# Optimization experiments

Measured on AMD Instinct MI355X. Metric: run time of the kernel, lower is better.

The kernel has to match this reference:

```python
import jax, jax.numpy as jnp
import numpy as np

B, T = 8, 8192
D_X, D_H, D_K, D_V = 256, 512, 128, 128
RES_DIMS = [128, 128, 128, 128]
R = sum(RES_DIMS)
MEM_SLOTS, EP_TOPK = 256, 8
LN_EPS = 1e-5


def _ln(x, g, b):
    m = x.mean(-1, keepdims=True)
    v = ((x - m) ** 2).mean(-1, keepdims=True)
    return (x - m) * jax.lax.rsqrt(v + LN_EPS) * g + b


def _l2norm(x, eps=1e-8):
    return x / jnp.maximum(jnp.linalg.norm(x, axis=-1, keepdims=True), eps)


def setup_inputs() -> dict:
    key = jax.random.key(0)
    ks = jax.random.split(key, 12)
    def w(k, shape):  # xavier-ish scaling
        return jax.random.normal(k, shape, jnp.float32) * (shape[-1] ** -0.5)
    return dict(
        x_seq=jax.random.normal(ks[0], (B, T, D_X), jnp.float32),
        Wx_w=w(ks[1], (R, D_X)), Wx_b=jnp.zeros((R,), jnp.float32),
        Wh_w=w(ks[2], (R, D_H)),
        res_alpha=jnp.full((len(RES_DIMS),), -1.0, jnp.float32),
        A_scale=jnp.ones((D_H,), jnp.float32),
        B_w=w(ks[3], (D_H, R)),
        U_w=w(ks[4], (D_H, D_X)), U_b=jnp.zeros((D_H,), jnp.float32),
        fftn_g=jnp.ones((D_H,), jnp.float32), fftn_b=jnp.zeros((D_H,), jnp.float32),
        fftp_w=w(ks[5], (D_H, D_H)), fftp_b=jnp.zeros((D_H,), jnp.float32),
        fft_mix=jnp.asarray(0.5, jnp.float32),
        mix_logit=jnp.asarray(0.0, jnp.float32),
        key_w=w(ks[6], (D_K, R + D_X)), key_b=jnp.zeros((D_K,), jnp.float32),
        val_w=w(ks[7], (D_V, D_H)), val_b=jnp.zeros((D_V,), jnp.float32),
        rm_w=w(ks[8], (D_H, D_V)), rm_b=jnp.zeros((D_H,), jnp.float32),
        rn_g=jnp.ones((R,), jnp.float32), rn_b=jnp.zeros((R,), jnp.float32),
        mem_keys=jax.random.normal(ks[9], (B, MEM_SLOTS, D_K), jnp.float32),
        mem_vals=jax.random.normal(ks[10], (B, MEM_SLOTS, D_K), jnp.float32),
        heb_H=jax.random.normal(ks[11], (B, D_K, D_V), jnp.float32) * 0.1,
    )


def reference(x_seq, Wx_w, Wx_b, Wh_w, res_alpha, A_scale, B_w, U_w, U_b,
              fftn_g, fftn_b, fftp_w, fftp_b, fft_mix, mix_logit,
              key_w, key_b, val_w, val_b, rm_w, rm_b, rn_g, rn_b,
              mem_keys, mem_vals, heb_H):
    b = x_seq.shape[0]
    seg_index = np.repeat(np.arange(len(RES_DIMS)), RES_DIMS)  # static (R,)
    h_prev = jnp.zeros((b, D_H), x_seq.dtype)  # h0 = None
    r_prev = jnp.zeros((b, R), x_seq.dtype)    # r0 = None

    # reservoir update (fully parallel over T since h_prev/r_prev are broadcast)
    Wx = jnp.einsum('btx,rx->btr', x_seq, Wx_w) + Wx_b
    Wh = (h_prev @ Wh_w.T)[:, None, :]                    # (B,1,R), no bias in fwd
    alpha = jax.nn.sigmoid(res_alpha)[seg_index]          # (R,)
    r_seq = alpha * r_prev[:, None, :] + (1.0 - alpha) * jnp.tanh(Wx + Wh)
    r_seq = _ln(r_seq, rn_g, rn_b)

    # core state
    Ah = A_scale * h_prev[:, None, :]
    Bh = jnp.einsum('btr,hr->bth', r_seq, B_w)
    Uh = jnp.einsum('btx,hx->bth', x_seq, U_w) + U_b
    h_tilde = jax.nn.gelu(Ah + Bh + Uh, approximate=False)

    # FFT feature mixing
    h_norm = _ln(h_tilde, fftn_g, fftn_b)
    s = jax.nn.sigmoid(fft_mix)
    h_freq = jnp.fft.rfft(h_norm, n=D_H, axis=-1, norm='ortho')
    h_ifft = jnp.fft.irfft(h_freq * s, n=D_H, axis=-1, norm='ortho')
    h_fft_out = jnp.einsum('bth,oh->bto', h_ifft, fftp_w) + fftp_b
    hs = (1.0 - s) * h_tilde + s * h_fft_out

    # memory recall (once per sequence, batched)
    k = jnp.einsum('btf,kf->btk', jnp.concatenate([r_seq, x_seq], axis=-1), key_w) + key_b
    v = jnp.einsum('bth,vh->btv', hs, val_w) + val_b  # as in original (used for auto_write)
    c = _l2norm(k)
    q = c.mean(axis=1)                                # (B,d_k)

    # episodic: cosine top-k over slots, softmax-weighted value read
    kn = _l2norm(mem_keys)
    sim = jnp.einsum('bk,bmk->bm', _l2norm(q), kn)
    top_sim, top_idx = jax.lax.top_k(sim, EP_TOPK)
    w_att = jax.nn.softmax(top_sim, axis=-1)
    vals = jnp.take_along_axis(mem_vals, top_idx[..., None], axis=1)  # (B,topk,d_v)
    v_hat = jnp.einsum('bk,bkv->bv', w_att, vals)

    # hebbian: linear associative read from per-batch outer-product memory
    v_hebb = jnp.einsum('bk,bkv->bv', q, heb_H)

    mix = jax.nn.sigmoid(mix_logit)
    v_comb = mix * v_hat + (1.0 - mix) * v_hebb
    h_mem = v_comb @ rm_w.T + rm_b                    # (B,d_h)
    hs = hs + 0.5 * h_mem[:, None, :]
    return hs, r_seq
```

## Files before the change

### kernel.cpp

```cpp
#include <hip/hip_runtime.h>
#include <cmath>


typedef __attribute__((ext_vector_type(8)))  short short8;
typedef __attribute__((ext_vector_type(16))) float f32x16;

__device__ __forceinline__ unsigned short f2bf(float f) {
  union { float f; unsigned u; } v; v.f = f;
  unsigned r = v.u + 0x7FFF + ((v.u >> 16) & 1);
  return (unsigned short)(r >> 16);
}
__device__ __forceinline__ float bf2f(unsigned short h) {
  union { unsigned u; float f; } v; v.u = ((unsigned)h) << 16; return v.f;
}
__device__ __forceinline__ f32x16 mfma16(short8 a, short8 b, f32x16 c) {
  return __builtin_amdgcn_mfma_f32_32x32x16_bf16(a, b, c, 0, 0, 0);
}
__device__ __forceinline__ void glds1k(const unsigned short* g, short* l, int lane) {
  typedef const __attribute__((address_space(1))) unsigned int* gp_t;
  typedef __attribute__((address_space(3))) unsigned int* lp_t;
  __builtin_amdgcn_global_load_lds((gp_t)(const void*)(g + lane * 8),
                                   (lp_t)(void*)l, 16, 0, 0);
}
__device__ __forceinline__ void barrier_lgkm() {
  asm volatile("s_waitcnt lgkmcnt(0)" ::: "memory");
  __builtin_amdgcn_s_barrier();
  __builtin_amdgcn_sched_barrier(0);
}

__global__ __launch_bounds__(256) void k_wconv(
    const float* __restrict__ wx, const float* __restrict__ key,
    const float* __restrict__ bw, const float* __restrict__ uw,
    const float* __restrict__ fftpw, const float* __restrict__ fg,
    unsigned short* __restrict__ wxp, unsigned short* __restrict__ keyp,
    unsigned short* __restrict__ bwp, unsigned short* __restrict__ uwp,
    unsigned short* __restrict__ fftps) {
  int i = blockIdx.x * 256 + threadIdx.x;
  if (i >= 884736) return;
  float v; int n, k, N; unsigned short* dst;
  if (i < 131072)      { int j = i;          N = 512; k = j & 255; n = j >> 8; v = wx[j];  dst = wxp; }
  else if (i < 229376) { int j = i - 131072; N = 128; k = j % 768; n = j / 768; v = key[j]; dst = keyp; }
  else if (i < 491520) { int j = i - 229376; N = 512; k = j & 511; n = j >> 9; v = bw[j];  dst = bwp; }
  else if (i < 622592) { int j = i - 491520; N = 512; k = j & 255; n = j >> 8; v = uw[j];  dst = uwp; }
  else                 { int j = i - 622592; N = 512; k = j & 511; n = j >> 9; v = fftpw[j] * fg[k]; dst = fftps; }
  dst[(k >> 5) * (N * 32) + ((k >> 3) & 3) * (N * 8) + n * 8 + (k & 7)] = f2bf(v);
}

__global__ __launch_bounds__(512, 4) void k_rseq(
    const float* __restrict__ x, const unsigned short* __restrict__ wxp,
    const float* __restrict__ wxb, const float* __restrict__ resa,
    const float* __restrict__ rng, const float* __restrict__ rnb,
    float* __restrict__ rout) {
  __shared__ short sA[2][1024];
  __shared__ float red[640];
  const int t = threadIdx.x, w = t >> 6, lane = t & 63, lr = lane & 31, lh = lane >> 5;
  const int m0 = blockIdx.x * 32;

  f32x16 acc[2];
#pragma unroll
  for (int ni = 0; ni < 2; ++ni)
#pragma unroll
    for (int e = 0; e < 16; ++e) acc[ni][e] = 0.f;

  short8 b0[4], b1[4];
  float2 a0, a1;

  auto loadB = [&](int sn, short8 (&bd)[4]) {
#pragma unroll
    for (int kh = 0; kh < 2; ++kh)
#pragma unroll
      for (int ni = 0; ni < 2; ++ni)
        bd[kh * 2 + ni] = *reinterpret_cast<const short8*>(
            wxp + (size_t)sn * 16384 + (kh * 2 + lh) * 4096 + (64 * w + 32 * ni + lr) * 8);
  };
  auto loadAct = [&](int sn, float2& ad) {
    int row = t >> 4, kq2 = t & 15;
    ad = *reinterpret_cast<const float2*>(x + (size_t)(m0 + row) * 256 + sn * 32 + kq2 * 2);
  };
  auto writeAct = [&](const float2& ad, int buf) {
    int row = t >> 4, kq2 = t & 15;
    unsigned p = (unsigned)f2bf(ad.x) | ((unsigned)f2bf(ad.y) << 16);
    *reinterpret_cast<unsigned*>(&sA[buf][(kq2 >> 2) * 256 + row * 8 + (kq2 & 3) * 2]) = p;
  };
  auto mfstep = [&](int buf, short8 (&bc)[4]) {
    short8 af[2];
#pragma unroll
    for (int kh = 0; kh < 2; ++kh)
      af[kh] = *reinterpret_cast<const short8*>(&sA[buf][(kh * 2 + lh) * 256 + lr * 8]);
    __builtin_amdgcn_s_setprio(1);
#pragma unroll
    for (int kh = 0; kh < 2; ++kh)
#pragma unroll
      for (int ni = 0; ni < 2; ++ni)
        acc[ni] = mfma16(af[kh], bc[kh * 2 + ni], acc[ni]);
    __builtin_amdgcn_s_setprio(0);
  };

  const int NS = 8;
  loadAct(0, a0);
  loadB(0, b0);
  loadAct(1, a1);
  writeAct(a0, 0);
  barrier_lgkm();
  for (int s = 0; s < NS; s += 2) {
    if (s + 1 < NS) loadB(s + 1, b1);
    if (s + 2 < NS) loadAct(s + 2, a0);
    mfstep(s & 1, b0);
    if (s + 1 < NS) writeAct(a1, (s + 1) & 1);
    barrier_lgkm();
    if (s + 2 < NS) loadB(s + 2, b0);
    if (s + 3 < NS) loadAct(s + 3, a1);
    mfstep((s + 1) & 1, b1);
    if (s + 2 < NS) writeAct(a0, s & 1);
    barrier_lgkm();
  }

#pragma unroll
  for (int ni = 0; ni < 2; ++ni) {
    int col = 64 * w + 32 * ni + lr;
    float al = 1.f / (1.f + expf(-resa[col >> 7]));
    float oma = 1.f - al, bbv = wxb[col];
#pragma unroll
    for (int r = 0; r < 16; ++r)
      acc[ni][r] = oma * tanhf(acc[ni][r] + bbv);
  }
#pragma unroll
  for (int r = 0; r < 16; ++r) {
    float s1 = acc[0][r] + acc[1][r];
    float s2 = acc[0][r] * acc[0][r] + acc[1][r] * acc[1][r];
#pragma unroll
    for (int m = 1; m <= 16; m <<= 1) { s1 += __shfl_xor(s1, m); s2 += __shfl_xor(s2, m); }
    int rl = (r & 3) + 8 * (r >> 2) + 4 * lh;
    if (lr == r) { red[w * 32 + rl] = s1; red[256 + w * 32 + rl] = s2; }
  }
  __syncthreads();
  if (t < 32) {
    float s1 = 0.f, s2 = 0.f;
#pragma unroll
    for (int n = 0; n < 8; ++n) { s1 += red[n * 32 + t]; s2 += red[256 + n * 32 + t]; }
    float mean = s1 * (1.f / 512.f);
    float var = s2 * (1.f / 512.f) - mean * mean;
    float rstd = rsqrtf(var + 1e-5f);
    red[512 + t * 2] = mean;
    red[512 + t * 2 + 1] = rstd;
  }
  __syncthreads();
#pragma unroll
  for (int q = 0; q < 4; ++q) {
    float4 stA = *reinterpret_cast<float4*>(&red[512 + (8 * q + 4 * lh) * 2]);
    float4 stB = *reinterpret_cast<float4*>(&red[512 + (8 * q + 4 * lh) * 2 + 4]);
    float mean[4] = {stA.x, stA.z, stB.x, stB.z};
    float rstd[4] = {stA.y, stA.w, stB.y, stB.w};
#pragma unroll
    for (int ni = 0; ni < 2; ++ni) {
      int col = 64 * w + 32 * ni + lr;
      float g = rng[col], bbv = rnb[col];
#pragma unroll
      for (int e = 0; e < 4; ++e) {
        int r = 4 * q + e;
        int grow = m0 + 8 * q + 4 * lh + e;
        rout[(size_t)grow * 512 + col] = (acc[ni][r] - mean[e]) * rstd[e] * g + bbv;
      }
    }
  }
}

__global__ __launch_bounds__(512, 2) void k_kq(
    const float* __restrict__ rseq, const float* __restrict__ x,
    const unsigned short* __restrict__ keyp, const float* __restrict__ keyb,
    float* __restrict__ partial) {
  __shared__ short sA[2][4096];
  const int t = threadIdx.x, w = t >> 6, lane = t & 63, lr = lane & 31, lh = lane >> 5;
  const int mw = w >> 1, nw = w & 1;
  const int m0 = blockIdx.x * 128;

  f32x16 acc[2];
#pragma unroll
  for (int ni = 0; ni < 2; ++ni)
#pragma unroll
    for (int e = 0; e < 16; ++e) acc[ni][e] = 0.f;

  short8 b0[4], b1[4];
  float4 a0[2], a1[2];

  auto loadB = [&](int sn, short8 (&bd)[4]) {
#pragma unroll
    for (int kh = 0; kh < 2; ++kh)
#pragma unroll
      for (int ni = 0; ni < 2; ++ni)
        bd[kh * 2 + ni] = *reinterpret_cast<const short8*>(
            keyp + (size_t)sn * 4096 + (kh * 2 + lh) * 1024 + (64 * nw + 32 * ni + lr) * 8);
  };
  auto loadAct = [&](int sn, float4 (&ad)[2]) {
    const float* src; int str, kb;
    if (sn < 16) { src = rseq; str = 512; kb = sn * 32; }
    else         { src = x;    str = 256; kb = (sn - 16) * 32; }
#pragma unroll
    for (int i = 0; i < 2; ++i) {
      int c = t + i * 512, row = c >> 3, kq = c & 7;
      ad[i] = *reinterpret_cast<const float4*>(src + (size_t)(m0 + row) * str + kb + kq * 4);
    }
  };
  auto writeAct = [&](const float4 (&ad)[2], int buf) {
#pragma unroll
    for (int i = 0; i < 2; ++i) {
      int c = t + i * 512, row = c >> 3, kq = c & 7;
      uint2 p;
      p.x = (unsigned)f2bf(ad[i].x) | ((unsigned)f2bf(ad[i].y) << 16);
      p.y = (unsigned)f2bf(ad[i].z) | ((unsigned)f2bf(ad[i].w) << 16);
      *reinterpret_cast<uint2*>(&sA[buf][(kq >> 1) * 1024 + row * 8 + (kq & 1) * 4]) = p;
    }
  };
  auto mfstep = [&](int buf, short8 (&bc)[4]) {
    short8 af[2];
#pragma unroll
    for (int kh = 0; kh < 2; ++kh)
      af[kh] = *reinterpret_cast<const short8*>(
          &sA[buf][(kh * 2 + lh) * 1024 + (32 * mw + lr) * 8]);
    __builtin_amdgcn_s_setprio(1);
#pragma unroll
    for (int kh = 0; kh < 2; ++kh)
#pragma unroll
      for (int ni = 0; ni < 2; ++ni)
        acc[ni] = mfma16(af[kh], bc[kh * 2 + ni], acc[ni]);
    __builtin_amdgcn_s_setprio(0);
  };

  const int NS = 24;
  loadAct(0, a0);
  loadB(0, b0);
  loadAct(1, a1);
  writeAct(a0, 0);
  barrier_lgkm();
  for (int s = 0; s < NS; s += 2) {
    if (s + 1 < NS) loadB(s + 1, b1);
    if (s + 2 < NS) loadAct(s + 2, a0);
    mfstep(s & 1, b0);
    if (s + 1 < NS) writeAct(a1, (s + 1) & 1);
    barrier_lgkm();
    if (s + 2 < NS) loadB(s + 2, b0);
    if (s + 3 < NS) loadAct(s + 3, a1);
    mfstep((s + 1) & 1, b1);
    if (s + 2 < NS) writeAct(a0, s & 1);
    barrier_lgkm();
  }

#pragma unroll
  for (int ni = 0; ni < 2; ++ni) {
    int col = 64 * nw + 32 * ni + lr;
    float bbv = keyb[col];
#pragma unroll
    for (int r = 0; r < 16; ++r) acc[ni][r] += bbv;
  }
  float* red = reinterpret_cast<float*>(sA);
#pragma unroll
  for (int r = 0; r < 16; ++r) {
    float s2 = acc[0][r] * acc[0][r] + acc[1][r] * acc[1][r];
#pragma unroll
    for (int m = 1; m <= 16; m <<= 1) s2 += __shfl_xor(s2, m);
    int rl = (r & 3) + 8 * (r >> 2) + 4 * lh;
    if (lr == r) red[(nw * 4 + mw) * 32 + rl] = s2;
  }
  __syncthreads();
  if (t < 128) {
    int ms = t >> 5, rl = t & 31;
    float s = red[(0 * 4 + ms) * 32 + rl] + red[(4 + ms) * 32 + rl];
    red[256 + ms * 32 + rl] = 1.f / fmaxf(sqrtf(s), 1e-8f);
  }
  __syncthreads();
  float p0 = 0.f, p1 = 0.f;
#pragma unroll
  for (int q = 0; q < 4; ++q) {
    float4 sc4 = *reinterpret_cast<float4*>(&red[256 + mw * 32 + 8 * q + 4 * lh]);
    float sc[4] = {sc4.x, sc4.y, sc4.z, sc4.w};
#pragma unroll
    for (int e = 0; e < 4; ++e) {
      int r = 4 * q + e;
      p0 += acc[0][r] * sc[e];
      p1 += acc[1][r] * sc[e];
    }
  }
  p0 += __shfl_xor(p0, 32);
  p1 += __shfl_xor(p1, 32);
  if (lh == 0) {
    red[384 + mw * 128 + 64 * nw + lr]      = p0;
    red[384 + mw * 128 + 64 * nw + 32 + lr] = p1;
  }
  __syncthreads();
  if (t < 128)
    partial[(size_t)blockIdx.x * 128 + t] =
        red[384 + t] + red[384 + 128 + t] + red[384 + 256 + t] + red[384 + 384 + t];
}

__global__ __launch_bounds__(256) void k_qred(const float* __restrict__ partial,
                                              float* __restrict__ q_ws) {
  int gid = blockIdx.x * 256 + threadIdx.x;
  int b = gid >> 7, c = gid & 127;
  float s = 0.f;
  for (int i = 0; i < 64; ++i) s += partial[(size_t)(b * 64 + i) * 128 + c];
  q_ws[gid] = s * (1.f / 8192.f);
}

__global__ __launch_bounds__(256) void k_cvec(const float* __restrict__ fb,
                                              const float* __restrict__ fftpw,
                                              float* __restrict__ cvec) {
  int o = blockIdx.x * 256 + threadIdx.x;
  const float* w = fftpw + (size_t)o * 512;
  float s = 0.f;
  for (int k = 0; k < 512; ++k) s += fb[k] * w[k];
  cvec[o] = s;
}

__global__ __launch_bounds__(256) void k_mem(
    const float* __restrict__ q_ws, const float* __restrict__ mkeys,
    const float* __restrict__ mvals, const float* __restrict__ hebH,
    const float* __restrict__ rmw, const float* __restrict__ rmb,
    const float* __restrict__ mixl, float* __restrict__ hm) {
  const int b = blockIdx.x, t = threadIdx.x;
  __shared__ float qv[128];
  __shared__ float ssim[256];
  __shared__ float red[256];
  __shared__ float tval[8];
  __shared__ int tidx[8];
  __shared__ float wsm[8];
  __shared__ float vcs[128];

  if (t < 128) qv[t] = q_ws[b * 128 + t];
  __syncthreads();
  red[t] = (t < 128) ? qv[t] * qv[t] : 0.f;
  __syncthreads();
  for (int s = 128; s > 0; s >>= 1) {
    if (t < s) red[t] += red[t + s];
    __syncthreads();
  }
  float qsc = 1.f / fmaxf(sqrtf(red[0]), 1e-8f);
  {
    const float* mk = mkeys + ((size_t)b * 256 + t) * 128;
    float dot = 0.f, ms = 0.f;
    for (int k = 0; k < 128; ++k) { float mv = mk[k]; dot += qv[k] * mv; ms += mv * mv; }
    ssim[t] = dot * qsc / fmaxf(sqrtf(ms), 1e-8f);
  }
  __syncthreads();
  for (int it = 0; it < 8; ++it) {
    if (t < 64) {
      float bv = -1e30f; int bi = 0;
#pragma unroll
      for (int u = 0; u < 4; ++u) {
        int m = t * 4 + u;
        float v = ssim[m];
        if (v > bv) { bv = v; bi = m; }
      }
      for (int off = 32; off; off >>= 1) {
        float ov = __shfl_xor(bv, off, 64);
        int oi = __shfl_xor(bi, off, 64);
        if (ov > bv || (ov == bv && oi < bi)) { bv = ov; bi = oi; }
      }
      if (t == 0) { tval[it] = bv; tidx[it] = bi; ssim[bi] = -1e30f; }
    }
    __syncthreads();
  }
  if (t == 0) {
    float m0 = tval[0], sum = 0.f, e[8];
#pragma unroll
    for (int i = 0; i < 8; ++i) { e[i] = expf(tval[i] - m0); sum += e[i]; }
#pragma unroll
    for (int i = 0; i < 8; ++i) wsm[i] = e[i] / sum;
  }
  __syncthreads();
  float mix = 1.f / (1.f + expf(-mixl[0]));
  if (t < 128) {
    float vh = 0.f;
#pragma unroll
    for (int i = 0; i < 8; ++i) vh += wsm[i] * mvals[((size_t)b * 256 + tidx[i]) * 128 + t];
    float vhb = 0.f;
    const float* H = hebH + (size_t)b * 128 * 128;
    for (int k = 0; k < 128; ++k) vhb += qv[k] * H[k * 128 + t];
    vcs[t] = mix * vh + (1.f - mix) * vhb;
  }
  __syncthreads();
  for (int h = t; h < 512; h += 256) {
    float sum = rmb[h];
    const float* wr = rmw + (size_t)h * 128;
    for (int v = 0; v < 128; ++v) sum += vcs[v] * wr[v];
    hm[b * 512 + h] = sum;
  }
}

__global__ __launch_bounds__(512, 4) void k_fused(
    const float* __restrict__ rseq, const float* __restrict__ x,
    const unsigned short* __restrict__ bwp, const unsigned short* __restrict__ uwp,
    const float* __restrict__ ub, const unsigned short* __restrict__ fftps,
    const float* __restrict__ fftpb, const float* __restrict__ fmix,
    const float* __restrict__ cvec, const float* __restrict__ hm,
    float* __restrict__ hs) {
  __shared__ short sA[2][1024];
  __shared__ short sH[16384];
  __shared__ float red[640];
  const int t = threadIdx.x, w = t >> 6, lane = t & 63, lr = lane & 31, lh = lane >> 5;
  const int m0 = blockIdx.x * 32;
  const int bidx = m0 >> 13;

  f32x16 acc[2];
#pragma unroll
  for (int ni = 0; ni < 2; ++ni)
#pragma unroll
    for (int e = 0; e < 16; ++e) acc[ni][e] = 0.f;

  short8 b0[4], b1[4];
  float2 a0, a1;

  auto loadB1 = [&](int sn, short8 (&bd)[4]) {
    const unsigned short* wp = (sn < 16) ? (bwp + (size_t)sn * 16384)
                                         : (uwp + (size_t)(sn - 16) * 16384);
#pragma unroll
    for (int kh = 0; kh < 2; ++kh)
#pragma unroll
      for (int ni = 0; ni < 2; ++ni)
        bd[kh * 2 + ni] = *reinterpret_cast<const short8*>(
            wp + (kh * 2 + lh) * 4096 + (64 * w + 32 * ni + lr) * 8);
  };
  auto loadAct = [&](int sn, float2& ad) {
    const float* src; int str, kb;
    if (sn < 16) { src = rseq; str = 512; kb = sn * 32; }
    else         { src = x;    str = 256; kb = (sn - 16) * 32; }
    int row = t >> 4, kq2 = t & 15;
    ad = *reinterpret_cast<const float2*>(src + (size_t)(m0 + row) * str + kb + kq2 * 2);
  };
  auto writeAct = [&](const float2& ad, int buf) {
    int row = t >> 4, kq2 = t & 15;
    unsigned p = (unsigned)f2bf(ad.x) | ((unsigned)f2bf(ad.y) << 16);
    *reinterpret_cast<unsigned*>(&sA[buf][(kq2 >> 2) * 256 + row * 8 + (kq2 & 3) * 2]) = p;
  };
  auto mfstep1 = [&](int buf, short8 (&bc)[4]) {
    short8 af[2];
#pragma unroll
    for (int kh = 0; kh < 2; ++kh)
      af[kh] = *reinterpret_cast<const short8*>(&sA[buf][(kh * 2 + lh) * 256 + lr * 8]);
    __builtin_amdgcn_s_setprio(1);
#pragma unroll
    for (int kh = 0; kh < 2; ++kh)
#pragma unroll
      for (int ni = 0; ni < 2; ++ni)
        acc[ni] = mfma16(af[kh], bc[kh * 2 + ni], acc[ni]);
    __builtin_amdgcn_s_setprio(0);
  };

  const int NS = 24;
  loadAct(0, a0);
  loadB1(0, b0);
  loadAct(1, a1);
  writeAct(a0, 0);
  barrier_lgkm();
  for (int s = 0; s < NS; s += 2) {
    if (s + 1 < NS) loadB1(s + 1, b1);
    if (s + 2 < NS) loadAct(s + 2, a0);
    mfstep1(s & 1, b0);
    if (s + 1 < NS) writeAct(a1, (s + 1) & 1);
    barrier_lgkm();
    if (s + 2 < NS) loadB1(s + 2, b0);
    if (s + 3 < NS) loadAct(s + 3, a1);
    mfstep1((s + 1) & 1, b1);
    if (s + 2 < NS) writeAct(a0, s & 1);
    barrier_lgkm();
  }

#pragma unroll
  for (int ni = 0; ni < 2; ++ni) {
    int col = 64 * w + 32 * ni + lr;
    float ubc = ub[col];
#pragma unroll
    for (int r = 0; r < 16; ++r) {
      float pre = acc[ni][r] + ubc;
      acc[ni][r] = 0.5f * pre * (1.f + erff(pre * 0.70710678118654752f));
    }
  }
#pragma unroll
  for (int r = 0; r < 16; ++r) {
    float s1 = acc[0][r] + acc[1][r];
    float s2 = acc[0][r] * acc[0][r] + acc[1][r] * acc[1][r];
#pragma unroll
    for (int m = 1; m <= 16; m <<= 1) { s1 += __shfl_xor(s1, m); s2 += __shfl_xor(s2, m); }
    int rl = (r & 3) + 8 * (r >> 2) + 4 * lh;
    if (lr == r) { red[w * 32 + rl] = s1; red[256 + w * 32 + rl] = s2; }
  }
  __syncthreads();
  if (t < 32) {
    float s1 = 0.f, s2 = 0.f;
#pragma unroll
    for (int n = 0; n < 8; ++n) { s1 += red[n * 32 + t]; s2 += red[256 + n * 32 + t]; }
    float mean = s1 * (1.f / 512.f);
    float var = s2 * (1.f / 512.f) - mean * mean;
    float rstd = rsqrtf(var + 1e-5f);
    red[512 + t * 2] = mean;
    red[512 + t * 2 + 1] = rstd;
  }
  __syncthreads();
  unsigned htp[2][8];
#pragma unroll
  for (int ni = 0; ni < 2; ++ni)
#pragma unroll
    for (int p = 0; p < 8; ++p)
      htp[ni][p] = (unsigned)f2bf(acc[ni][2 * p]) |
                   ((unsigned)f2bf(acc[ni][2 * p + 1]) << 16);
  auto loadB2 = [&](int sn, short8 (&bd)[4]) {
#pragma unroll
    for (int kh = 0; kh < 2; ++kh)
#pragma unroll
      for (int ni = 0; ni < 2; ++ni)
        bd[kh * 2 + ni] = *reinterpret_cast<const short8*>(
            fftps + (size_t)sn * 16384 + (kh * 2 + lh) * 4096 + (64 * w + 32 * ni + lr) * 8);
  };
  loadB2(0, b0);
#pragma unroll
  for (int q = 0; q < 4; ++q) {
    float4 stA = *reinterpret_cast<float4*>(&red[512 + (8 * q + 4 * lh) * 2]);
    float4 stB = *reinterpret_cast<float4*>(&red[512 + (8 * q + 4 * lh) * 2 + 4]);
    float mean[4] = {stA.x, stA.z, stB.x, stB.z};
    float rstd[4] = {stA.y, stA.w, stB.y, stB.w};
#pragma unroll
    for (int ni = 0; ni < 2; ++ni) {
      int col = 64 * w + 32 * ni + lr;
#pragma unroll
      for (int e = 0; e < 4; ++e) {
        int r = 4 * q + e;
        float z = (acc[ni][r] - mean[e]) * rstd[e];
        int rloc = 8 * q + 4 * lh + e;
        sH[(col >> 3) * 256 + rloc * 8 + (col & 7)] = (short)f2bf(z);
      }
    }
  }
#pragma unroll
  for (int ni = 0; ni < 2; ++ni)
#pragma unroll
    for (int e = 0; e < 16; ++e) acc[ni][e] = 0.f;
  barrier_lgkm();

  auto mfstep2 = [&](int slotbase, short8 (&bc)[4]) {
    short8 af[2];
#pragma unroll
    for (int kh = 0; kh < 2; ++kh)
      af[kh] = *reinterpret_cast<const short8*>(
          &sH[(slotbase + kh * 2 + lh) * 256 + lr * 8]);
    __builtin_amdgcn_s_setprio(1);
#pragma unroll
    for (int kh = 0; kh < 2; ++kh)
#pragma unroll
      for (int ni = 0; ni < 2; ++ni)
        acc[ni] = mfma16(af[kh], bc[kh * 2 + ni], acc[ni]);
    __builtin_amdgcn_s_setprio(0);
  };
  for (int s = 0; s < 16; s += 2) {
    loadB2(s + 1, b1);
    mfstep2(s * 4, b0);
    if (s + 2 < 16) loadB2(s + 2, b0);
    mfstep2((s + 1) * 4, b1);
  }

  const float sg = 1.f / (1.f + expf(-fmix[0]));
  const float s2f = sg * sg, oms = 1.f - sg;
#pragma unroll
  for (int ni = 0; ni < 2; ++ni) {
    int col = 64 * w + 32 * ni + lr;
    float base = s2f * cvec[col] + sg * fftpb[col] + 0.5f * hm[bidx * 512 + col];
#pragma unroll
    for (int p = 0; p < 8; ++p) {
      unsigned pk = htp[ni][p];
      int r0 = 2 * p;
      int rloc = (r0 & 3) + 8 * (r0 >> 2) + 4 * lh;
      float o0 = oms * bf2f((unsigned short)(pk & 0xFFFF)) + s2f * acc[ni][r0] + base;
      float o1 = oms * bf2f((unsigned short)(pk >> 16)) + s2f * acc[ni][r0 + 1] + base;
      hs[(size_t)(m0 + rloc) * 512 + col] = o0;
      hs[(size_t)(m0 + rloc + 1) * 512 + col] = o1;
    }
  }
}

extern "C" void kernel_launch(void* const* d_in, const int* in_sizes, int n_in,
                              void* d_out, int out_size, void* d_ws, size_t ws_size,
                              hipStream_t stream) {
  (void)in_sizes; (void)n_in; (void)out_size; (void)ws_size;
  const float* x     = (const float*)d_in[0];
  const float* Wxw   = (const float*)d_in[1];
  const float* Wxb   = (const float*)d_in[2];
  const float* resa  = (const float*)d_in[4];
  const float* Bw    = (const float*)d_in[6];
  const float* Uw    = (const float*)d_in[7];
  const float* Ub    = (const float*)d_in[8];
  const float* fg    = (const float*)d_in[9];
  const float* fb    = (const float*)d_in[10];
  const float* fftpw = (const float*)d_in[11];
  const float* fftpb = (const float*)d_in[12];
  const float* fmix  = (const float*)d_in[13];
  const float* mixl  = (const float*)d_in[14];
  const float* keyw  = (const float*)d_in[15];
  const float* keyb  = (const float*)d_in[16];
  const float* rmw   = (const float*)d_in[19];
  const float* rmb   = (const float*)d_in[20];
  const float* rng   = (const float*)d_in[21];
  const float* rnb   = (const float*)d_in[22];
  const float* mkeys = (const float*)d_in[23];
  const float* mvals = (const float*)d_in[24];
  const float* hebH  = (const float*)d_in[25];

  float* outp = (float*)d_out;
  float* hs   = outp;
  float* rout = outp + (size_t)65536 * 512;

  unsigned short* wsu = (unsigned short*)d_ws;
  unsigned short* wxp    = wsu;
  unsigned short* keyp   = wsu + 131072;
  unsigned short* bwp    = wsu + 229376;
  unsigned short* uwp    = wsu + 491520;
  unsigned short* fftps  = wsu + 622592;
  float* wsf     = (float*)d_ws;
  float* partial = wsf + 524288;
  float* q_ws    = wsf + 589824;
  float* hm      = wsf + 590848;
  float* cvec    = wsf + 594944;

  k_wconv<<<3456, 256, 0, stream>>>(Wxw, keyw, Bw, Uw, fftpw, fg,
                                    wxp, keyp, bwp, uwp, fftps);
  k_cvec <<<2,    256, 0, stream>>>(fb, fftpw, cvec);
  k_rseq <<<2048, 512, 0, stream>>>(x, wxp, Wxb, resa, rng, rnb, rout);
  k_kq   <<<512,  512, 0, stream>>>(rout, x, keyp, keyb, partial);
  k_qred <<<4,    256, 0, stream>>>(partial, q_ws);
  k_mem  <<<8,    256, 0, stream>>>(q_ws, mkeys, mvals, hebH, rmw, rmb, mixl, hm);
  k_fused<<<2048, 512, 0, stream>>>(rout, x, bwp, uwp, Ub, fftps, fftpb,
                                    fmix, cvec, hm, hs);
}
```

Before: 311.7 us.

## Fuse key projection into r_seq kernel and stage full activation tiles in LDS

Merges the r_seq GEMM and the key/query-partial GEMM into one kernel. The normalized r tile is kept in LDS as bf16 and reused with the x tile for the key projection, so r_seq no longer has to be re-read from global memory. The fused main kernel also loads its whole 32-row r and x tiles into LDS up front, replacing the double-buffered per-step staging and its barriers. In exchange, LDS use per block rises, which may reduce occupancy, and the partial-sum buffer grows four-fold, so the q reduction now loops over 256 partials instead of 64.

```diff
diff --git a/kernel.cpp b/kernel.cpp
--- a/kernel.cpp
+++ b/kernel.cpp
@@ -15,12 +15,6 @@
 }
 __device__ __forceinline__ f32x16 mfma16(short8 a, short8 b, f32x16 c) {
   return __builtin_amdgcn_mfma_f32_32x32x16_bf16(a, b, c, 0, 0, 0);
-}
-__device__ __forceinline__ void glds1k(const unsigned short* g, short* l, int lane) {
-  typedef const __attribute__((address_space(1))) unsigned int* gp_t;
-  typedef __attribute__((address_space(3))) unsigned int* lp_t;
-  __builtin_amdgcn_global_load_lds((gp_t)(const void*)(g + lane * 8),
-                                   (lp_t)(void*)l, 16, 0, 0);
 }
 __device__ __forceinline__ void barrier_lgkm() {
   asm volatile("s_waitcnt lgkmcnt(0)" ::: "memory");
@@ -46,47 +40,50 @@
   dst[(k >> 5) * (N * 32) + ((k >> 3) & 3) * (N * 8) + n * 8 + (k & 7)] = f2bf(v);
 }
 
-__global__ __launch_bounds__(512, 4) void k_rseq(
+__global__ __launch_bounds__(512, 4) void k_rk(
     const float* __restrict__ x, const unsigned short* __restrict__ wxp,
+    const unsigned short* __restrict__ keyp,
     const float* __restrict__ wxb, const float* __restrict__ resa,
     const float* __restrict__ rng, const float* __restrict__ rnb,
-    float* __restrict__ rout) {
-  __shared__ short sA[2][1024];
+    const float* __restrict__ keyb,
+    float* __restrict__ rout, float* __restrict__ partial) {
+  __shared__ short sX[8192];
+  __shared__ short sR[16384];
   __shared__ float red[640];
   const int t = threadIdx.x, w = t >> 6, lane = t & 63, lr = lane & 31, lh = lane >> 5;
   const int m0 = blockIdx.x * 32;
 
+#pragma unroll
+  for (int i = 0; i < 4; ++i) {
+    int c = t + i * 512;
+    int row = c >> 6, k0 = (c & 63) * 4;
+    float4 v = *reinterpret_cast<const float4*>(x + (size_t)(m0 + row) * 256 + k0);
+    uint2 p;
+    p.x = (unsigned)f2bf(v.x) | ((unsigned)f2bf(v.y) << 16);
+    p.y = (unsigned)f2bf(v.z) | ((unsigned)f2bf(v.w) << 16);
+    *reinterpret_cast<uint2*>(&sX[(k0 >> 3) * 256 + row * 8 + (k0 & 7)]) = p;
+  }
+  barrier_lgkm();
+
   f32x16 acc[2];
 #pragma unroll
   for (int ni = 0; ni < 2; ++ni)
 #pragma unroll
     for (int e = 0; e < 16; ++e) acc[ni][e] = 0.f;
-
   short8 b0[4], b1[4];
-  float2 a0, a1;
-
-  auto loadB = [&](int sn, short8 (&bd)[4]) {
+  auto loadB0 = [&](int s, short8 (&bd)[4]) {
 #pragma unroll
     for (int kh = 0; kh < 2; ++kh)
 #pragma unroll
       for (int ni = 0; ni < 2; ++ni)
         bd[kh * 2 + ni] = *reinterpret_cast<const short8*>(
-            wxp + (size_t)sn * 16384 + (kh * 2 + lh) * 4096 + (64 * w + 32 * ni + lr) * 8);
-  };
-  auto loadAct = [&](int sn, float2& ad) {
-    int row = t >> 4, kq2 = t & 15;
-    ad = *reinterpret_cast<const float2*>(x + (size_t)(m0 + row) * 256 + sn * 32 + kq2 * 2);
-  };
-  auto writeAct = [&](const float2& ad, int buf) {
-    int row = t >> 4, kq2 = t & 15;
-    unsigned p = (unsigned)f2bf(ad.x) | ((unsigned)f2bf(ad.y) << 16);
-    *reinterpret_cast<unsigned*>(&sA[buf][(kq2 >> 2) * 256 + row * 8 + (kq2 & 3) * 2]) = p;
-  };
-  auto mfstep = [&](int buf, short8 (&bc)[4]) {
+            wxp + (size_t)s * 16384 + (kh * 2 + lh) * 4096 + (64 * w + 32 * ni + lr) * 8);
+  };
+  auto mf0 = [&](int s, short8 (&bc)[4]) {
     short8 af[2];
 #pragma unroll
     for (int kh = 0; kh < 2; ++kh)
-      af[kh] = *reinterpret_cast<const short8*>(&sA[buf][(kh * 2 + lh) * 256 + lr * 8]);
+      af[kh] = *reinterpret_cast<const short8*>(&sX[(s * 4 + kh * 2 + lh) * 256 + lr * 8]);
     __builtin_amdgcn_s_setprio(1);
 #pragma unroll
     for (int kh = 0; kh < 2; ++kh)
@@ -95,24 +92,12 @@
         acc[ni] = mfma16(af[kh], bc[kh * 2 + ni], acc[ni]);
     __builtin_amdgcn_s_setprio(0);
   };
-
-  const int NS = 8;
-  loadAct(0, a0);
-  loadB(0, b0);
-  loadAct(1, a1);
-  writeAct(a0, 0);
-  barrier_lgkm();
-  for (int s = 0; s < NS; s += 2) {
-    if (s + 1 < NS) loadB(s + 1, b1);
-    if (s + 2 < NS) loadAct(s + 2, a0);
-    mfstep(s & 1, b0);
-    if (s + 1 < NS) writeAct(a1, (s + 1) & 1);
-    barrier_lgkm();
-    if (s + 2 < NS) loadB(s + 2, b0);
-    if (s + 3 < NS) loadAct(s + 3, a1);
-    mfstep((s + 1) & 1, b1);
-    if (s + 2 < NS) writeAct(a0, s & 1);
-    barrier_lgkm();
+  loadB0(0, b0);
+  for (int s = 0; s < 8; s += 2) {
+    loadB0(s + 1, b1);
+    mf0(s, b0);
+    if (s + 2 < 8) loadB0(s + 2, b0);
+    mf0(s + 1, b1);
   }
 
 #pragma unroll
@@ -158,138 +143,77 @@
 #pragma unroll
       for (int e = 0; e < 4; ++e) {
         int r = 4 * q + e;
-        int grow = m0 + 8 * q + 4 * lh + e;
-        rout[(size_t)grow * 512 + col] = (acc[ni][r] - mean[e]) * rstd[e] * g + bbv;
+        int rloc = 8 * q + 4 * lh + e;
+        float val = (acc[ni][r] - mean[e]) * rstd[e] * g + bbv;
+        rout[(size_t)(m0 + rloc) * 512 + col] = val;
+        sR[(col >> 3) * 256 + rloc * 8 + (col & 7)] = (short)f2bf(val);
       }
     }
   }
-}
-
-__global__ __launch_bounds__(512, 2) void k_kq(
-    const float* __restrict__ rseq, const float* __restrict__ x,
-    const unsigned short* __restrict__ keyp, const float* __restrict__ keyb,
-    float* __restrict__ partial) {
-  __shared__ short sA[2][4096];
-  const int t = threadIdx.x, w = t >> 6, lane = t & 63, lr = lane & 31, lh = lane >> 5;
-  const int mw = w >> 1, nw = w & 1;
-  const int m0 = blockIdx.x * 128;
-
-  f32x16 acc[2];
-#pragma unroll
-  for (int ni = 0; ni < 2; ++ni)
-#pragma unroll
-    for (int e = 0; e < 16; ++e) acc[ni][e] = 0.f;
-
-  short8 b0[4], b1[4];
-  float4 a0[2], a1[2];
-
-  auto loadB = [&](int sn, short8 (&bd)[4]) {
-#pragma unroll
-    for (int kh = 0; kh < 2; ++kh)
-#pragma unroll
-      for (int ni = 0; ni < 2; ++ni)
-        bd[kh * 2 + ni] = *reinterpret_cast<const short8*>(
-            keyp + (size_t)sn * 4096 + (kh * 2 + lh) * 1024 + (64 * nw + 32 * ni + lr) * 8);
-  };
-  auto loadAct = [&](int sn, float4 (&ad)[2]) {
-    const float* src; int str, kb;
-    if (sn < 16) { src = rseq; str = 512; kb = sn * 32; }
-    else         { src = x;    str = 256; kb = (sn - 16) * 32; }
-#pragma unroll
-    for (int i = 0; i < 2; ++i) {
-      int c = t + i * 512, row = c >> 3, kq = c & 7;
-      ad[i] = *reinterpret_cast<const float4*>(src + (size_t)(m0 + row) * str + kb + kq * 4);
+  barrier_lgkm();
+
+  const int g = w >> 2, nw2 = w & 3;
+  f32x16 ak;
+#pragma unroll
+  for (int e = 0; e < 16; ++e) ak[e] = 0.f;
+  short8 kb0[2], kb1[2];
+  auto loadBk = [&](int gc, short8 (&bd)[2]) {
+#pragma unroll
+    for (int kh = 0; kh < 2; ++kh)
+      bd[kh] = *reinterpret_cast<const short8*>(
+          keyp + (size_t)gc * 4096 + (kh * 2 + lh) * 1024 + (32 * nw2 + lr) * 8);
+  };
+  auto mfk = [&](int gc, short8 (&bc)[2]) {
+    const short* P = (gc < 16) ? sR : sX;
+    int sb = (gc < 16) ? gc * 4 : (gc - 16) * 4;
+    short8 af[2];
+#pragma unroll
+    for (int kh = 0; kh < 2; ++kh)
+      af[kh] = *reinterpret_cast<const short8*>(&P[(sb + kh * 2 + lh) * 256 + lr * 8]);
+    __builtin_amdgcn_s_setprio(1);
+#pragma unroll
+    for (int kh = 0; kh < 2; ++kh)
+      ak = mfma16(af[kh], bc[kh], ak);
+    __builtin_amdgcn_s_setprio(0);
+  };
+  const int gbase = g * 12;
+  loadBk(gbase, kb0);
+  for (int s = 0; s < 12; s += 2) {
+    loadBk(gbase + s + 1, kb1);
+    mfk(gbase + s, kb0);
+    if (s + 2 < 12) loadBk(gbase + s + 2, kb0);
+    mfk(gbase + s + 1, kb1);
+  }
+  __syncthreads();
+  float* kp = reinterpret_cast<float*>(sR);
+#pragma unroll
+  for (int r = 0; r < 16; ++r) {
+    int rr = (r & 3) + 8 * (r >> 2) + 4 * lh;
+    kp[g * 4096 + rr * 128 + nw2 * 32 + lr] = ak[r];
+  }
+  __syncthreads();
+  {
+    int rr = t >> 4, cg = t & 15;
+    float s1 = 0.f;
+#pragma unroll
+    for (int j = 0; j < 8; ++j) {
+      int c = cg * 8 + j;
+      float v = kp[rr * 128 + c] + kp[4096 + rr * 128 + c] + keyb[c];
+      s1 += v * v;
     }
-  };
-  auto writeAct = [&](const float4 (&ad)[2], int buf) {
-#pragma unroll
-    for (int i = 0; i < 2; ++i) {
-      int c = t + i * 512, row = c >> 3, kq = c & 7;
-      uint2 p;
-      p.x = (unsigned)f2bf(ad[i].x) | ((unsigned)f2bf(ad[i].y) << 16);
-      p.y = (unsigned)f2bf(ad[i].z) | ((unsigned)f2bf(ad[i].w) << 16);
-      *reinterpret_cast<uint2*>(&sA[buf][(kq >> 1) * 1024 + row * 8 + (kq & 1) * 4]) = p;
-    }
-  };
-  auto mfstep = [&](int buf, short8 (&bc)[4]) {
-    short8 af[2];
-#pragma unroll
-    for (int kh = 0; kh < 2; ++kh)
-      af[kh] = *reinterpret_cast<const short8*>(
-          &sA[buf][(kh * 2 + lh) * 1024 + (32 * mw + lr) * 8]);
-    __builtin_amdgcn_s_setprio(1);
-#pragma unroll
-    for (int kh = 0; kh < 2; ++kh)
-#pragma unroll
-      for (int ni = 0; ni < 2; ++ni)
-        acc[ni] = mfma16(af[kh], bc[kh * 2 + ni], acc[ni]);
-    __builtin_amdgcn_s_setprio(0);
-  };
-
-  const int NS = 24;
-  loadAct(0, a0);
-  loadB(0, b0);
-  loadAct(1, a1);
-  writeAct(a0, 0);
-  barrier_lgkm();
-  for (int s = 0; s < NS; s += 2) {
-    if (s + 1 < NS) loadB(s + 1, b1);
-    if (s + 2 < NS) loadAct(s + 2, a0);
-    mfstep(s & 1, b0);
-    if (s + 1 < NS) writeAct(a1, (s + 1) & 1);
-    barrier_lgkm();
-    if (s + 2 < NS) loadB(s + 2, b0);
-    if (s + 3 < NS) loadAct(s + 3, a1);
-    mfstep((s + 1) & 1, b1);
-    if (s + 2 < NS) writeAct(a0, s & 1);
-    barrier_lgkm();
-  }
-
-#pragma unroll
-  for (int ni = 0; ni < 2; ++ni) {
-    int col = 64 * nw + 32 * ni + lr;
-    float bbv = keyb[col];
-#pragma unroll
-    for (int r = 0; r < 16; ++r) acc[ni][r] += bbv;
-  }
-  float* red = reinterpret_cast<float*>(sA);
-#pragma unroll
-  for (int r = 0; r < 16; ++r) {
-    float s2 = acc[0][r] * acc[0][r] + acc[1][r] * acc[1][r];
-#pragma unroll
-    for (int m = 1; m <= 16; m <<= 1) s2 += __shfl_xor(s2, m);
-    int rl = (r & 3) + 8 * (r >> 2) + 4 * lh;
-    if (lr == r) red[(nw * 4 + mw) * 32 + rl] = s2;
+#pragma unroll
+    for (int m = 1; m <= 8; m <<= 1) s1 += __shfl_xor(s1, m);
+    if (cg == 0) red[rr] = 1.f / fmaxf(sqrtf(s1), 1e-8f);
   }
   __syncthreads();
   if (t < 128) {
-    int ms = t >> 5, rl = t & 31;
-    float s = red[(0 * 4 + ms) * 32 + rl] + red[(4 + ms) * 32 + rl];
-    red[256 + ms * 32 + rl] = 1.f / fmaxf(sqrtf(s), 1e-8f);
-  }
-  __syncthreads();
-  float p0 = 0.f, p1 = 0.f;
-#pragma unroll
-  for (int q = 0; q < 4; ++q) {
-    float4 sc4 = *reinterpret_cast<float4*>(&red[256 + mw * 32 + 8 * q + 4 * lh]);
-    float sc[4] = {sc4.x, sc4.y, sc4.z, sc4.w};
-#pragma unroll
-    for (int e = 0; e < 4; ++e) {
-      int r = 4 * q + e;
-      p0 += acc[0][r] * sc[e];
-      p1 += acc[1][r] * sc[e];
-    }
-  }
-  p0 += __shfl_xor(p0, 32);
-  p1 += __shfl_xor(p1, 32);
-  if (lh == 0) {
-    red[384 + mw * 128 + 64 * nw + lr]      = p0;
-    red[384 + mw * 128 + 64 * nw + 32 + lr] = p1;
-  }
-  __syncthreads();
-  if (t < 128)
-    partial[(size_t)blockIdx.x * 128 + t] =
-        red[384 + t] + red[384 + 128 + t] + red[384 + 256 + t] + red[384 + 384 + t];
+    float p = 0.f;
+    float bb = keyb[t];
+#pragma unroll 4
+    for (int rr = 0; rr < 32; ++rr)
+      p += (kp[rr * 128 + t] + kp[4096 + rr * 128 + t] + bb) * red[rr];
+    partial[(size_t)blockIdx.x * 128 + t] = p;
+  }
 }
 
 __global__ __launch_bounds__(256) void k_qred(const float* __restrict__ partial,
@@ -297,7 +221,7 @@
   int gid = blockIdx.x * 256 + threadIdx.x;
   int b = gid >> 7, c = gid & 127;
   float s = 0.f;
-  for (int i = 0; i < 64; ++i) s += partial[(size_t)(b * 64 + i) * 128 + c];
+  for (int i = 0; i < 256; ++i) s += partial[(size_t)(b * 256 + i) * 128 + c];
   q_ws[gid] = s * (1.f / 8192.f);
 }
 
@@ -393,25 +317,44 @@
     const float* __restrict__ fftpb, const float* __restrict__ fmix,
     const float* __restrict__ cvec, const float* __restrict__ hm,
     float* __restrict__ hs) {
-  __shared__ short sA[2][1024];
-  __shared__ short sH[16384];
+  __shared__ short sX[8192];
+  __shared__ short sR[16384];
   __shared__ float red[640];
   const int t = threadIdx.x, w = t >> 6, lane = t & 63, lr = lane & 31, lh = lane >> 5;
   const int m0 = blockIdx.x * 32;
   const int bidx = m0 >> 13;
 
+#pragma unroll
+  for (int i = 0; i < 8; ++i) {
+    int c = t + i * 512;
+    int row = c >> 7, k0 = (c & 127) * 4;
+    float4 v = *reinterpret_cast<const float4*>(rseq + (size_t)(m0 + row) * 512 + k0);
+    uint2 p;
+    p.x = (unsigned)f2bf(v.x) | ((unsigned)f2bf(v.y) << 16);
+    p.y = (unsigned)f2bf(v.z) | ((unsigned)f2bf(v.w) << 16);
+    *reinterpret_cast<uint2*>(&sR[(k0 >> 3) * 256 + row * 8 + (k0 & 7)]) = p;
+  }
+#pragma unroll
+  for (int i = 0; i < 4; ++i) {
+    int c = t + i * 512;
+    int row = c >> 6, k0 = (c & 63) * 4;
+    float4 v = *reinterpret_cast<const float4*>(x + (size_t)(m0 + row) * 256 + k0);
+    uint2 p;
+    p.x = (unsigned)f2bf(v.x) | ((unsigned)f2bf(v.y) << 16);
+    p.y = (unsigned)f2bf(v.z) | ((unsigned)f2bf(v.w) << 16);
+    *reinterpret_cast<uint2*>(&sX[(k0 >> 3) * 256 + row * 8 + (k0 & 7)]) = p;
+  }
+  barrier_lgkm();
+
   f32x16 acc[2];
 #pragma unroll
   for (int ni = 0; ni < 2; ++ni)
 #pragma unroll
     for (int e = 0; e < 16; ++e) acc[ni][e] = 0.f;
-
   short8 b0[4], b1[4];
-  float2 a0, a1;
-
-  auto loadB1 = [&](int sn, short8 (&bd)[4]) {
-    const unsigned short* wp = (sn < 16) ? (bwp + (size_t)sn * 16384)
-                                         : (uwp + (size_t)(sn - 16) * 16384);
+  auto loadB1 = [&](int s, short8 (&bd)[4]) {
+    const unsigned short* wp = (s < 16) ? (bwp + (size_t)s * 16384)
+                                        : (uwp + (size_t)(s - 16) * 16384);
 #pragma unroll
     for (int kh = 0; kh < 2; ++kh)
 #pragma unroll
@@ -419,23 +362,13 @@
         bd[kh * 2 + ni] = *reinterpret_cast<const short8*>(
             wp + (kh * 2 + lh) * 4096 + (64 * w + 32 * ni + lr) * 8);
   };
-  auto loadAct = [&](int sn, float2& ad) {
-    const float* src; int str, kb;
-    if (sn < 16) { src = rseq; str = 512; kb = sn * 32; }
-    else         { src = x;    str = 256; kb = (sn - 16) * 32; }
-    int row = t >> 4, kq2 = t & 15;
-    ad = *reinterpret_cast<const float2*>(src + (size_t)(m0 + row) * str + kb + kq2 * 2);
-  };
-  auto writeAct = [&](const float2& ad, int buf) {
-    int row = t >> 4, kq2 = t & 15;
-    unsigned p = (unsigned)f2bf(ad.x) | ((unsigned)f2bf(ad.y) << 16);
-    *reinterpret_cast<unsigned*>(&sA[buf][(kq2 >> 2) * 256 + row * 8 + (kq2 & 3) * 2]) = p;
-  };
-  auto mfstep1 = [&](int buf, short8 (&bc)[4]) {
+  auto mf1 = [&](int s, short8 (&bc)[4]) {
+    const short* P = (s < 16) ? sR : sX;
+    int sb = (s < 16) ? s * 4 : (s - 16) * 4;
     short8 af[2];
 #pragma unroll
     for (int kh = 0; kh < 2; ++kh)
-      af[kh] = *reinterpret_cast<const short8*>(&sA[buf][(kh * 2 + lh) * 256 + lr * 8]);
+      af[kh] = *reinterpret_cast<const short8*>(&P[(sb + kh * 2 + lh) * 256 + lr * 8]);
     __builtin_amdgcn_s_setprio(1);
 #pragma unroll
     for (int kh = 0; kh < 2; ++kh)
@@ -444,24 +377,12 @@
         acc[ni] = mfma16(af[kh], bc[kh * 2 + ni], acc[ni]);
     __builtin_amdgcn_s_setprio(0);
   };
-
-  const int NS = 24;
-  loadAct(0, a0);
   loadB1(0, b0);
-  loadAct(1, a1);
-  writeAct(a0, 0);
-  barrier_lgkm();
-  for (int s = 0; s < NS; s += 2) {
-    if (s + 1 < NS) loadB1(s + 1, b1);
-    if (s + 2 < NS) loadAct(s + 2, a0);
-    mfstep1(s & 1, b0);
-    if (s + 1 < NS) writeAct(a1, (s + 1) & 1);
-    barrier_lgkm();
-    if (s + 2 < NS) loadB1(s + 2, b0);
-    if (s + 3 < NS) loadAct(s + 3, a1);
-    mfstep1((s + 1) & 1, b1);
-    if (s + 2 < NS) writeAct(a0, s & 1);
-    barrier_lgkm();
+  for (int s = 0; s < 24; s += 2) {
+    loadB1(s + 1, b1);
+    mf1(s, b0);
+    if (s + 2 < 24) loadB1(s + 2, b0);
+    mf1(s + 1, b1);
   }
 
 #pragma unroll
@@ -502,13 +423,13 @@
     for (int p = 0; p < 8; ++p)
       htp[ni][p] = (unsigned)f2bf(acc[ni][2 * p]) |
                    ((unsigned)f2bf(acc[ni][2 * p + 1]) << 16);
-  auto loadB2 = [&](int sn, short8 (&bd)[4]) {
+  auto loadB2 = [&](int s, short8 (&bd)[4]) {
 #pragma unroll
     for (int kh = 0; kh < 2; ++kh)
 #pragma unroll
       for (int ni = 0; ni < 2; ++ni)
         bd[kh * 2 + ni] = *reinterpret_cast<const short8*>(
-            fftps + (size_t)sn * 16384 + (kh * 2 + lh) * 4096 + (64 * w + 32 * ni + lr) * 8);
+            fftps + (size_t)s * 16384 + (kh * 2 + lh) * 4096 + (64 * w + 32 * ni + lr) * 8);
   };
   loadB2(0, b0);
 #pragma unroll
@@ -525,7 +446,7 @@
         int r = 4 * q + e;
         float z = (acc[ni][r] - mean[e]) * rstd[e];
         int rloc = 8 * q + 4 * lh + e;
-        sH[(col >> 3) * 256 + rloc * 8 + (col & 7)] = (short)f2bf(z);
+        sR[(col >> 3) * 256 + rloc * 8 + (col & 7)] = (short)f2bf(z);
       }
     }
   }
@@ -535,12 +456,11 @@
     for (int e = 0; e < 16; ++e) acc[ni][e] = 0.f;
   barrier_lgkm();
 
-  auto mfstep2 = [&](int slotbase, short8 (&bc)[4]) {
+  auto mf2 = [&](int s, short8 (&bc)[4]) {
     short8 af[2];
 #pragma unroll
     for (int kh = 0; kh < 2; ++kh)
-      af[kh] = *reinterpret_cast<const short8*>(
-          &sH[(slotbase + kh * 2 + lh) * 256 + lr * 8]);
+      af[kh] = *reinterpret_cast<const short8*>(&sR[(s * 4 + kh * 2 + lh) * 256 + lr * 8]);
     __builtin_amdgcn_s_setprio(1);
 #pragma unroll
     for (int kh = 0; kh < 2; ++kh)
@@ -551,9 +471,9 @@
   };
   for (int s = 0; s < 16; s += 2) {
     loadB2(s + 1, b1);
-    mfstep2(s * 4, b0);
+    mf2(s, b0);
     if (s + 2 < 16) loadB2(s + 2, b0);
-    mfstep2((s + 1) * 4, b1);
+    mf2(s + 1, b1);
   }
 
   const float sg = 1.f / (1.f + expf(-fmix[0]));
@@ -614,15 +534,15 @@
   unsigned short* fftps  = wsu + 622592;
   float* wsf     = (float*)d_ws;
   float* partial = wsf + 524288;
-  float* q_ws    = wsf + 589824;
-  float* hm      = wsf + 590848;
-  float* cvec    = wsf + 594944;
+  float* q_ws    = wsf + 786432;
+  float* hm      = wsf + 787456;
+  float* cvec    = wsf + 791552;
 
   k_wconv<<<3456, 256, 0, stream>>>(Wxw, keyw, Bw, Uw, fftpw, fg,
                                     wxp, keyp, bwp, uwp, fftps);
   k_cvec <<<2,    256, 0, stream>>>(fb, fftpw, cvec);
-  k_rseq <<<2048, 512, 0, stream>>>(x, wxp, Wxb, resa, rng, rnb, rout);
-  k_kq   <<<512,  512, 0, stream>>>(rout, x, keyp, keyb, partial);
+  k_rk   <<<2048, 512, 0, stream>>>(x, wxp, keyp, Wxb, resa, rng, rnb, keyb,
+                                    rout, partial);
   k_qred <<<4,    256, 0, stream>>>(partial, q_ws);
   k_mem  <<<8,    256, 0, stream>>>(q_ws, mkeys, mvals, hebH, rmw, rmb, mixl, hm);
   k_fused<<<2048, 512, 0, stream>>>(rout, x, bwp, uwp, Ub, fftps, fftpb,
```

Result: no change. 309.0 us (-0.9%).
